# Kernel optimization log

Measured on AMD Instinct MI355X. Metric: run time of the kernel, lower is better.

## Reference

```python
import jax, jax.numpy as jnp
import numpy as np

NUM_HEADS = 16
HIDDEN = 1152
MLP = 4304
HEAD_DIM = HIDDEN // NUM_HEADS  # 72
SEQ = 3072
LN_EPS = 1e-5


def setup_inputs() -> dict:
    key = jax.random.key(0)
    ks = jax.random.split(key, 16)
    inv = 1.0 / np.sqrt(HIDDEN)
    inv_m = 1.0 / np.sqrt(MLP)
    pos = jnp.arange(SEQ, dtype=jnp.float32)[:, None]
    freq = jnp.exp(-jnp.arange(HEAD_DIM // 2, dtype=jnp.float32) * (np.log(10000.0) / (HEAD_DIM // 2)))
    ang = pos * freq[None, :]
    return {
        "hidden_states": jax.random.normal(ks[0], (SEQ, HIDDEN), jnp.float32),
        "rope_cos": jnp.cos(ang),
        "rope_sin": jnp.sin(ang),
        "ln0_g": jnp.ones((HIDDEN,), jnp.float32),
        "ln0_b": jnp.zeros((HIDDEN,), jnp.float32),
        "ln1_g": jnp.ones((HIDDEN,), jnp.float32),
        "ln1_b": jnp.zeros((HIDDEN,), jnp.float32),
        "wqkv_w": jax.random.normal(ks[1], (3 * HIDDEN, HIDDEN), jnp.float32) * inv,
        "wqkv_b": jnp.zeros((3 * HIDDEN,), jnp.float32),
        "wo_w": jax.random.normal(ks[2], (HIDDEN, HIDDEN), jnp.float32) * inv,
        "wo_b": jnp.zeros((HIDDEN,), jnp.float32),
        "fc0_w": jax.random.normal(ks[3], (MLP, HIDDEN), jnp.float32) * inv,
        "fc0_b": jnp.zeros((MLP,), jnp.float32),
        "fc1_w": jax.random.normal(ks[4], (HIDDEN, MLP), jnp.float32) * inv_m,
        "fc1_b": jnp.zeros((HIDDEN,), jnp.float32),
    }


def _layernorm(x, g, b):
    mu = jnp.mean(x, axis=-1, keepdims=True)
    var = jnp.mean(jnp.square(x - mu), axis=-1, keepdims=True)
    return (x - mu) * jax.lax.rsqrt(var + LN_EPS) * g + b


def _apply_rope(x, cos, sin):
    # x: [S, H, Dh]; cos/sin: [S, Dh/2]
    xp = x.astype(jnp.float32).reshape(*x.shape[:-1], -1, 2)  # [S, H, Dh/2, 2]
    xr, xi = xp[..., 0], xp[..., 1]
    c = cos[:, None, :]
    s = sin[:, None, :]
    out_r = xr * c - xi * s
    out_i = xr * s + xi * c
    return jnp.stack([out_r, out_i], axis=-1).reshape(x.shape).astype(x.dtype)


def reference(hidden_states, rope_cos, rope_sin, ln0_g, ln0_b, ln1_g, ln1_b,
              wqkv_w, wqkv_b, wo_w, wo_b, fc0_w, fc0_b, fc1_w, fc1_b):
    S = hidden_states.shape[0]
    residual = hidden_states
    h = _layernorm(hidden_states, ln0_g, ln0_b)
    xqkv = (h @ wqkv_w.T + wqkv_b).reshape(S, 3, NUM_HEADS, HEAD_DIM)
    xq, xk, xv = xqkv[:, 0], xqkv[:, 1], xqkv[:, 2]
    xq = _apply_rope(xq, rope_cos, rope_sin)
    xk = _apply_rope(xk, rope_cos, rope_sin)
    scale = 1.0 / np.sqrt(HEAD_DIM)
    scores = jnp.einsum('shd,thd->hst', xq, xk) * scale  # [H, S, S]
    attn = jax.nn.softmax(scores.astype(jnp.float32), axis=-1).astype(xq.dtype)
    out = jnp.einsum('hst,thd->shd', attn, xv).reshape(S, HIDDEN)
    h = residual + (out @ wo_w.T + wo_b)
    residual = h
    h = _layernorm(h, ln1_g, ln1_b)
    h = jax.nn.gelu(h @ fc0_w.T + fc0_b, approximate=True)
    h = h @ fc1_w.T + fc1_b
    return residual + h
```

## Files before the change

kernel.cpp:

```cpp
#include <hip/hip_runtime.h>
#include <hip/hip_bf16.h>
#include <math.h>

typedef __hip_bfloat16 bf16;
typedef __attribute__((ext_vector_type(8))) short short8;
typedef __attribute__((ext_vector_type(4))) short short4v;
typedef __attribute__((ext_vector_type(4))) float f32x4;

#define SEQ 3072
#define HID 1152
#define NHEAD 16
#define HD 72
#define HDP 96
#define MLPD 4304
#define MLPP 4352

__device__ __forceinline__ void async_lds16(void* lds, const void* g) {
  __builtin_amdgcn_global_load_lds((const __attribute__((address_space(1))) void*)g,
                                   (__attribute__((address_space(3))) void*)lds,
                                   16, 0, 0);
}

__device__ __forceinline__ unsigned cvt_pk2(float a, float b) {
  unsigned r;
  asm("v_cvt_pk_bf16_f32 %0, %1, %2" : "=v"(r) : "v"(a), "v"(b));
  return r;
}

__device__ __forceinline__ float exp2a(float x) {
  float r;
  asm("v_exp_f32 %0, %1" : "=v"(r) : "v"(x));
  return r;
}

__global__ __launch_bounds__(256) void cast_bf16_k(const float* __restrict__ in,
                                                   unsigned* __restrict__ out2, int n4) {
  int stride = gridDim.x * blockDim.x;
  for (int i = blockIdx.x * blockDim.x + threadIdx.x; i < n4; i += stride) {
    float4 u = ((const float4*)in)[i];
    uint2 w = make_uint2(cvt_pk2(u.x, u.y), cvt_pk2(u.z, u.w));
    ((uint2*)out2)[i] = w;
  }
}

__global__ __launch_bounds__(256) void cast_pad_rows_k(const float* __restrict__ in,
                                                       unsigned* __restrict__ out2,
                                                       int R, int C4, int n4) {
  int stride = gridDim.x * blockDim.x;
  for (int i = blockIdx.x * blockDim.x + threadIdx.x; i < n4; i += stride) {
    int r = i / C4;
    uint2 w = make_uint2(0u, 0u);
    if (r < R) {
      float4 u = ((const float4*)in)[i];
      w = make_uint2(cvt_pk2(u.x, u.y), cvt_pk2(u.z, u.w));
    }
    ((uint2*)out2)[i] = w;
  }
}

__global__ __launch_bounds__(256) void cast_pad_cols_k(const float* __restrict__ in,
                                                       unsigned* __restrict__ out2,
                                                       int C4, int Cp4, int n4) {
  int stride = gridDim.x * blockDim.x;
  for (int i = blockIdx.x * blockDim.x + threadIdx.x; i < n4; i += stride) {
    int r = i / Cp4, c4 = i - r * Cp4;
    uint2 w = make_uint2(0u, 0u);
    if (c4 < C4) {
      float4 u = ((const float4*)in)[r * C4 + c4];
      w = make_uint2(cvt_pk2(u.x, u.y), cvt_pk2(u.z, u.w));
    }
    ((uint2*)out2)[i] = w;
  }
}

__global__ __launch_bounds__(256) void ln_k(const float* __restrict__ x,
                                            const float* __restrict__ g,
                                            const float* __restrict__ b,
                                            bf16* __restrict__ o) {
  int row = blockIdx.x;
  const float4* xr = (const float4*)(x + (size_t)row * HID);
  float sum = 0.f, sq = 0.f;
  for (int c = threadIdx.x; c < HID / 4; c += 256) {
    float4 u = xr[c];
    sum += u.x + u.y + u.z + u.w;
    sq += u.x * u.x + u.y * u.y + u.z * u.z + u.w * u.w;
  }
#pragma unroll
  for (int off = 32; off > 0; off >>= 1) {
    sum += __shfl_down(sum, off, 64);
    sq += __shfl_down(sq, off, 64);
  }
  __shared__ float red[8];
  int wv = threadIdx.x >> 6;
  if ((threadIdx.x & 63) == 0) { red[wv] = sum; red[4 + wv] = sq; }
  __syncthreads();
  if (threadIdx.x == 0) {
    red[0] = red[0] + red[1] + red[2] + red[3];
    red[4] = red[4] + red[5] + red[6] + red[7];
  }
  __syncthreads();
  float mu = red[0] * (1.f / HID);
  float var = red[4] * (1.f / HID) - mu * mu;
  float inv = rsqrtf(var + 1e-5f);
  uint2* o4 = (uint2*)(o + (size_t)row * HID);
  const float4* g4 = (const float4*)g;
  const float4* b4 = (const float4*)b;
  for (int c = threadIdx.x; c < HID / 4; c += 256) {
    float4 u = xr[c], gg = g4[c], bb = b4[c];
    uint2 w = make_uint2(cvt_pk2((u.x - mu) * inv * gg.x + bb.x, (u.y - mu) * inv * gg.y + bb.y),
                         cvt_pk2((u.z - mu) * inv * gg.z + bb.z, (u.w - mu) * inv * gg.w + bb.w));
    o4[c] = w;
  }
}

template <int EPI>
__global__ __launch_bounds__(256) void gemm_bf16(const bf16* __restrict__ A,
                                                 const bf16* __restrict__ Bt,
                                                 const float* __restrict__ bias, int nbias,
                                                 const float* __restrict__ res,
                                                 float* __restrict__ outf,
                                                 bf16* __restrict__ outb,
                                                 int M, int N, int K) {
  __shared__ bf16 As[3][128 * 32];
  __shared__ bf16 Bs[3][128 * 32];
  const int t = threadIdx.x;
  const int l = t & 63;
  const int w = t >> 6;
  const int wr = w >> 1, wc = w & 1;
  const int lrow = l & 15;
  const int lk = (l >> 4) * 8;
  const int wg = (blockIdx.x & 7) * (gridDim.x >> 3) + (blockIdx.x >> 3);
  const int gyt = M >> 7;
  const int xt = wg / gyt;
  const int yt = wg - xt * gyt;
  const int m0 = yt * 128;
  const int n0 = xt * 128;
  const int arow = t >> 2;
  const int ach = (t & 3) * 8;

  const bf16* pa0 = &A[(size_t)(m0 + arow) * K + ach];
  const bf16* pa1 = &A[(size_t)(m0 + arow + 64) * K + ach];
  const bf16* pb0 = &Bt[(size_t)(n0 + arow) * K + ach];
  const bf16* pb1 = &Bt[(size_t)(n0 + arow + 64) * K + ach];
  auto STAGE = [&](int buf, int kt) {
    size_t off = (size_t)kt * 32;
    async_lds16(&As[buf][t * 8], pa0 + off);
    async_lds16(&As[buf][(256 + t) * 8], pa1 + off);
    async_lds16(&Bs[buf][t * 8], pb0 + off);
    async_lds16(&Bs[buf][(256 + t) * 8], pb1 + off);
  };

  f32x4 acc[4][4] = {};
  const int nkt = K >> 5;
  STAGE(0, 0);
  STAGE(1, 1);
  int bcur = 0;
  for (int kt = 0; kt < nkt; ++kt) {
    if (kt + 1 < nkt) {
      asm volatile("s_waitcnt vmcnt(4)" ::: "memory");
    } else {
      asm volatile("s_waitcnt vmcnt(0)" ::: "memory");
    }
    __builtin_amdgcn_s_barrier();
    int bn2 = bcur + 2;
    if (bn2 >= 3) bn2 -= 3;
    if (kt + 2 < nkt) STAGE(bn2, kt + 2);

    short8 af[4], bfr[4];
#pragma unroll
    for (int i = 0; i < 4; ++i)
      af[i] = *(const short8*)&As[bcur][(wr * 64 + i * 16 + lrow) * 32 + lk];
#pragma unroll
    for (int i = 0; i < 4; ++i)
      bfr[i] = *(const short8*)&Bs[bcur][(wc * 64 + i * 16 + lrow) * 32 + lk];
    __builtin_amdgcn_s_setprio(1);
#pragma unroll
    for (int i = 0; i < 4; ++i)
#pragma unroll
      for (int j = 0; j < 4; ++j)
        acc[i][j] = __builtin_amdgcn_mfma_f32_16x16x32_bf16(af[i], bfr[j], acc[i][j], 0, 0, 0);
    __builtin_amdgcn_s_setprio(0);
    ++bcur;
    if (bcur == 3) bcur = 0;
  }

#pragma unroll
  for (int i = 0; i < 4; ++i) {
    int rowb = m0 + wr * 64 + i * 16 + (l >> 4) * 4;
#pragma unroll
    for (int j = 0; j < 4; ++j) {
      int col = n0 + wc * 64 + j * 16 + lrow;
      float bv = (col < nbias) ? bias[col] : 0.f;
#pragma unroll
      for (int r2 = 0; r2 < 4; ++r2) {
        size_t idx = (size_t)(rowb + r2) * N + col;
        float v = acc[i][j][r2] + bv;
        if (EPI == 0) {
          outf[idx] = v;
        } else if (EPI == 1) {
          outf[idx] = v + res[idx];
        } else {
          float u = 0.7978845608028654f * (v + 0.044715f * v * v * v);
          u = fminf(fmaxf(u, -15.f), 15.f);
          float tt = __expf(2.f * u);
          outb[idx] = __float2bfloat16(v * tt / (tt + 1.f));
        }
      }
    }
  }
}

__global__ __launch_bounds__(256) void rope_split(const float* __restrict__ xqkv,
                                                  const float* __restrict__ cosb,
                                                  const float* __restrict__ sinb,
                                                  bf16* __restrict__ qp,
                                                  bf16* __restrict__ kp,
                                                  bf16* __restrict__ vt) {
  __shared__ bf16 vl[64][72];
  const int t = threadIdx.x;
  const int h = blockIdx.y;
  const int s0 = blockIdx.x * 64;
  const float scale = 0.17002445f;
  for (int idx = t; idx < 64 * 48; idx += 256) {
    int sl = idx / 48, pi = idx - sl * 48;
    int srow = s0 + sl;
    size_t obase = ((size_t)h * SEQ + srow) * HDP + 2 * pi;
    if (pi < 36) {
      const float* xr = xqkv + (size_t)srow * (3 * HID) + h * HD + 2 * pi;
      float qr = xr[0], qi = xr[1];
      float kr = xr[HID], ki = xr[HID + 1];
      float c = cosb[srow * 36 + pi], sn = sinb[srow * 36 + pi];
      *(unsigned*)&qp[obase] = cvt_pk2((qr * c - qi * sn) * scale, (qr * sn + qi * c) * scale);
      *(unsigned*)&kp[obase] = cvt_pk2(kr * c - ki * sn, kr * sn + ki * c);
    } else {
      *(unsigned*)&qp[obase] = 0u;
      *(unsigned*)&kp[obase] = 0u;
    }
  }
  for (int idx = t; idx < 64 * 72; idx += 256) {
    int sl = idx / 72, d = idx - sl * 72;
    vl[sl][d] = __float2bfloat16(xqkv[(size_t)(s0 + sl) * (3 * HID) + 2 * HID + h * HD + d]);
  }
  __syncthreads();
  bf16 z = __float2bfloat16(0.f);
  for (int idx = t; idx < HDP * 64; idx += 256) {
    int d = idx / 64, sl = idx - d * 64;
    vt[((size_t)h * HDP + d) * SEQ + s0 + sl] = (d < 72) ? vl[sl][d] : z;
  }
}

__global__ __launch_bounds__(128) void flash_attn(const bf16* __restrict__ q,
                                                  const bf16* __restrict__ kk,
                                                  const bf16* __restrict__ vT,
                                                  bf16* __restrict__ o) {
  __shared__ alignas(16) bf16 KV3[3 * 6144];
  __shared__ alignas(16) bf16 Pl[2][2][512];
  const int t = threadIdx.x;
  const int l = t & 63;
  const int w = t >> 6;
  const int g = l >> 4;
  const int lrow = l & 15;
  const int bid = blockIdx.x;
  const int kq = bid >> 3;
  const int h = (bid & 7) * 2 + (kq & 1);
  const int q0 = (kq >> 1) * 64 + w * 32;
  const int NT = SEQ / 32;

  const bf16* sbase[6];
  int smul[6];
#pragma unroll
  for (int i = 0; i < 6; ++i) {
    int s = t + i * 128;
    if (s < 384) {
      int cb = s >> 5, kv = s & 31;
      sbase[i] = kk + ((size_t)h * SEQ + kv) * HDP + cb * 8;
      smul[i] = 32 * HDP;
    } else {
      int vs = s - 384;
      int cb = vs / 96, d = vs - cb * 96;
      sbase[i] = vT + ((size_t)h * HDP + d) * SEQ + cb * 8;
      smul[i] = 32;
    }
  }
  auto STAGE = [&](int tile, int bufOff) {
#pragma unroll
    for (int i = 0; i < 6; ++i)
      async_lds16(&KV3[bufOff + (t + i * 128) * 8], sbase[i] + (size_t)tile * smul[i]);
  };

  short8 qf[2][3];
#pragma unroll
  for (int ss = 0; ss < 2; ++ss)
#pragma unroll
    for (int f = 0; f < 3; ++f)
      qf[ss][f] =
          *(const short8*)&q[((size_t)h * SEQ + q0 + ss * 16 + lrow) * HDP + f * 32 + g * 8];

  float m_r[2] = {-1e30f, -1e30f};
  float l_r[2] = {0.f, 0.f};
  f32x4 oa0[5] = {}, oa1[5] = {};

  STAGE(0, 0);
  STAGE(1, 6144);
  STAGE(2, 12288);
  asm volatile("s_waitcnt vmcnt(12)" ::: "memory");
  __builtin_amdgcn_s_barrier();

  f32x4 stA[2][2] = {}, stB[2][2];
  int b0 = 0;
#pragma unroll
  for (int nf = 0; nf < 2; ++nf)
#pragma unroll
    for (int f = 0; f < 3; ++f) {
      short8 kfrag = *(const short8*)&KV3[0 + (f * 4 + g) * 256 + (nf * 16 + lrow) * 8];
      stA[0][nf] = __builtin_amdgcn_mfma_f32_16x16x32_bf16(kfrag, qf[0][f], stA[0][nf], 0, 0, 0);
      stA[1][nf] = __builtin_amdgcn_mfma_f32_16x16x32_bf16(kfrag, qf[1][f], stA[1][nf], 0, 0, 0);
    }

  auto SOFTMAX = [&](f32x4* st, float& mr, float& lr, f32x4* oav, int ss) {
    float pmax = fmaxf(fmaxf(fmaxf(st[0][0], st[0][1]), fmaxf(st[0][2], st[0][3])),
                       fmaxf(fmaxf(st[1][0], st[1][1]), fmaxf(st[1][2], st[1][3])));
    if (!__all(pmax - mr <= 11.54f)) {
      float rm = pmax;
      rm = fmaxf(rm, __shfl_xor(rm, 16, 64));
      rm = fmaxf(rm, __shfl_xor(rm, 32, 64));
      float mn = fmaxf(mr, rm);
      float alpha = exp2a(mr - mn);
      lr *= alpha;
#pragma unroll
      for (int nf = 0; nf < 5; ++nf)
#pragma unroll
        for (int r = 0; r < 4; ++r) oav[nf][r] *= alpha;
      mr = mn;
    }
#pragma unroll
    for (int nf = 0; nf < 2; ++nf)
#pragma unroll
      for (int r = 0; r < 4; ++r) st[nf][r] = exp2a(st[nf][r] - mr);
    lr += (st[0][0] + st[0][1]) + (st[0][2] + st[0][3]) +
          (st[1][0] + st[1][1]) + (st[1][2] + st[1][3]);
#pragma unroll
    for (int nf = 0; nf < 2; ++nf) {
      uint2* dst = (uint2*)&Pl[w][ss][(2 * nf + (g >> 1)) * 128 + lrow * 8 + (g & 1) * 4];
      *dst = make_uint2(cvt_pk2(st[nf][0], st[nf][1]), cvt_pk2(st[nf][2], st[nf][3]));
    }
  };

  for (int kt = 0; kt < NT - 1; ++kt) {
    int b1 = b0 + 6144;
    if (b1 == 18432) b1 = 0;
    asm volatile("s_waitcnt vmcnt(6)" ::: "memory");
    __builtin_amdgcn_s_barrier();

#pragma unroll
    for (int s2 = 0; s2 < 2; ++s2)
#pragma unroll
      for (int nf = 0; nf < 2; ++nf) stB[s2][nf] = (f32x4){0.f, 0.f, 0.f, 0.f};
    __builtin_amdgcn_s_setprio(1);
#pragma unroll
    for (int nf = 0; nf < 2; ++nf)
#pragma unroll
      for (int f = 0; f < 3; ++f) {
        short8 kfrag = *(const short8*)&KV3[b1 + (f * 4 + g) * 256 + (nf * 16 + lrow) * 8];
        stB[0][nf] = __builtin_amdgcn_mfma_f32_16x16x32_bf16(kfrag, qf[0][f], stB[0][nf], 0, 0, 0);
        stB[1][nf] = __builtin_amdgcn_mfma_f32_16x16x32_bf16(kfrag, qf[1][f], stB[1][nf], 0, 0, 0);
      }
    __builtin_amdgcn_s_setprio(0);

    SOFTMAX(stA[0], m_r[0], l_r[0], oa0, 0);
    SOFTMAX(stA[1], m_r[1], l_r[1], oa1, 1);

    {
      short8 pa0 = *(const short8*)&Pl[w][0][g * 128 + lrow * 8];
      short8 pa1 = *(const short8*)&Pl[w][1][g * 128 + lrow * 8];
      __builtin_amdgcn_s_setprio(1);
#pragma unroll
      for (int nf = 0; nf < 5; ++nf) {
        short8 bv = *(const short8*)&KV3[b0 + 3072 + g * 768 + (nf * 16 + lrow) * 8];
        oa0[nf] = __builtin_amdgcn_mfma_f32_16x16x32_bf16(bv, pa0, oa0[nf], 0, 0, 0);
        oa1[nf] = __builtin_amdgcn_mfma_f32_16x16x32_bf16(bv, pa1, oa1[nf], 0, 0, 0);
      }
      __builtin_amdgcn_s_setprio(0);
    }

    asm volatile("s_waitcnt lgkmcnt(0)" ::: "memory");
    __builtin_amdgcn_s_barrier();
    int s = kt + 3;
    if (s >= NT) s -= NT;
    STAGE(s, b0);
#pragma unroll
    for (int s2 = 0; s2 < 2; ++s2)
#pragma unroll
      for (int nf = 0; nf < 2; ++nf) stA[s2][nf] = stB[s2][nf];
    b0 = b1;
  }

  SOFTMAX(stA[0], m_r[0], l_r[0], oa0, 0);
  SOFTMAX(stA[1], m_r[1], l_r[1], oa1, 1);
  {
    short8 pa0 = *(const short8*)&Pl[w][0][g * 128 + lrow * 8];
    short8 pa1 = *(const short8*)&Pl[w][1][g * 128 + lrow * 8];
#pragma unroll
    for (int nf = 0; nf < 5; ++nf) {
      short8 bv = *(const short8*)&KV3[b0 + 3072 + g * 768 + (nf * 16 + lrow) * 8];
      oa0[nf] = __builtin_amdgcn_mfma_f32_16x16x32_bf16(bv, pa0, oa0[nf], 0, 0, 0);
      oa1[nf] = __builtin_amdgcn_mfma_f32_16x16x32_bf16(bv, pa1, oa1[nf], 0, 0, 0);
    }
  }

#pragma unroll
  for (int ss = 0; ss < 2; ++ss) {
    f32x4* oav = ss ? oa1 : oa0;
    float lt = l_r[ss];
    lt += __shfl_xor(lt, 16, 64);
    lt += __shfl_xor(lt, 32, 64);
    float rcp = 1.f / lt;
    size_t obase = (size_t)(q0 + ss * 16 + lrow) * HID + h * HD;
#pragma unroll
    for (int nf = 0; nf < 5; ++nf) {
      int d = nf * 16 + g * 4;
      if (d + 3 < HD) {
        uint2 pk = make_uint2(cvt_pk2(oav[nf][0] * rcp, oav[nf][1] * rcp),
                              cvt_pk2(oav[nf][2] * rcp, oav[nf][3] * rcp));
        *(uint2*)&o[obase + d] = pk;
      }
    }
  }
}

extern "C" void kernel_launch(void* const* d_in, const int* in_sizes, int n_in,
                              void* d_out, int out_size, void* d_ws, size_t ws_size,
                              hipStream_t stream) {
  (void)in_sizes; (void)n_in; (void)out_size;
  const float* hidden = (const float*)d_in[0];
  const float* cosb = (const float*)d_in[1];
  const float* sinb = (const float*)d_in[2];
  const float* ln0g = (const float*)d_in[3];
  const float* ln0b = (const float*)d_in[4];
  const float* ln1g = (const float*)d_in[5];
  const float* ln1b = (const float*)d_in[6];
  const float* wqkv = (const float*)d_in[7];
  const float* bqkv = (const float*)d_in[8];
  const float* wo = (const float*)d_in[9];
  const float* bo = (const float*)d_in[10];
  const float* w0 = (const float*)d_in[11];
  const float* b0 = (const float*)d_in[12];
  const float* w1 = (const float*)d_in[13];
  const float* b1 = (const float*)d_in[14];

  char* p = (char*)d_ws;
  auto alloc = [&](size_t n) {
    char* r = p;
    p += (n + 255) & ~(size_t)255;
    return r;
  };
  bf16* wqkv_bf = (bf16*)alloc((size_t)3 * HID * HID * 2);
  bf16* wo_bf = (bf16*)alloc((size_t)HID * HID * 2);
  bf16* fc0_bf = (bf16*)alloc((size_t)MLPP * HID * 2);
  bf16* fc1_bf = (bf16*)alloc((size_t)HID * MLPP * 2);
  bf16* ln0_bf = (bf16*)alloc((size_t)SEQ * HID * 2);
  float* xqkv = (float*)alloc((size_t)SEQ * 3 * HID * 4);
  bf16* qp = (bf16*)alloc((size_t)NHEAD * SEQ * HDP * 2);
  bf16* kp = (bf16*)alloc((size_t)NHEAD * SEQ * HDP * 2);
  bf16* vt = (bf16*)alloc((size_t)NHEAD * HDP * SEQ * 2);
  bf16* attn_bf = (bf16*)alloc((size_t)SEQ * HID * 2);
  float* h1 = (float*)alloc((size_t)SEQ * HID * 4);
  bf16* ln1_bf = (bf16*)alloc((size_t)SEQ * HID * 2);
  bf16* gelu_bf = (bf16*)alloc((size_t)SEQ * MLPP * 2);
  if ((size_t)(p - (char*)d_ws) > ws_size) return;

  dim3 blk(256);
  cast_bf16_k<<<2048, blk, 0, stream>>>(wqkv, (unsigned*)wqkv_bf, 3 * HID * HID / 4);
  cast_bf16_k<<<1024, blk, 0, stream>>>(wo, (unsigned*)wo_bf, HID * HID / 4);
  cast_pad_rows_k<<<2048, blk, 0, stream>>>(w0, (unsigned*)fc0_bf, MLPD, HID / 4, MLPP * HID / 4);
  cast_pad_cols_k<<<2048, blk, 0, stream>>>(w1, (unsigned*)fc1_bf, MLPD / 4, MLPP / 4, HID * MLPP / 4);
  ln_k<<<SEQ, blk, 0, stream>>>(hidden, ln0g, ln0b, ln0_bf);
  gemm_bf16<0><<<dim3((3 * HID / 128) * (SEQ / 128)), blk, 0, stream>>>(
      ln0_bf, wqkv_bf, bqkv, 3 * HID, nullptr, xqkv, nullptr, SEQ, 3 * HID, HID);
  rope_split<<<dim3(SEQ / 64, NHEAD), blk, 0, stream>>>(xqkv, cosb, sinb, qp, kp, vt);
  flash_attn<<<dim3(768), dim3(128), 0, stream>>>(qp, kp, vt, attn_bf);
  gemm_bf16<1><<<dim3((HID / 128) * (SEQ / 128)), blk, 0, stream>>>(
      attn_bf, wo_bf, bo, HID, hidden, h1, nullptr, SEQ, HID, HID);
  ln_k<<<SEQ, blk, 0, stream>>>(h1, ln1g, ln1b, ln1_bf);
  gemm_bf16<2><<<dim3((MLPP / 128) * (SEQ / 128)), blk, 0, stream>>>(
      ln1_bf, fc0_bf, b0, MLPD, nullptr, nullptr, gelu_bf, SEQ, MLPP, HID);
  gemm_bf16<1><<<dim3((HID / 128) * (SEQ / 128)), blk, 0, stream>>>(
      gelu_bf, fc1_bf, b1, HID, h1, (float*)d_out, nullptr, SEQ, HID, MLPP);
}
```

Measured before the change: 399.9 us.

## Restructure flash attention to 6 waves × 16 rows with 64-wide KV tiles

The flash attention kernel moves from 2 waves each handling 32 query rows with 32-key tiles to 6 waves each handling 16 query rows with 64-key tiles. K and V get separate LDS buffers, triple-buffered for K and double-buffered for V, and the grid drops to 512 blocks of 384 threads. The aim is more reuse of each staged KV tile across query rows and fewer loop iterations and barriers. In exchange each wave keeps fewer query rows in flight, and a larger block coordinates on every barrier.

```diff
diff --git a/kernel.cpp b/kernel.cpp
--- a/kernel.cpp
+++ b/kernel.cpp
@@ -249,12 +249,13 @@
   }
 }
 
-__global__ __launch_bounds__(128) void flash_attn(const bf16* __restrict__ q,
+__global__ __launch_bounds__(384) void flash_attn(const bf16* __restrict__ q,
                                                   const bf16* __restrict__ kk,
                                                   const bf16* __restrict__ vT,
                                                   bf16* __restrict__ o) {
-  __shared__ alignas(16) bf16 KV3[3 * 6144];
-  __shared__ alignas(16) bf16 Pl[2][2][512];
+  __shared__ alignas(16) bf16 Ks[3][6144];
+  __shared__ alignas(16) bf16 Vs[2][6144];
+  __shared__ alignas(16) bf16 Pl[6][1024];
   const int t = threadIdx.x;
   const int l = t & 63;
   const int w = t >> 6;
@@ -263,167 +264,147 @@
   const int bid = blockIdx.x;
   const int kq = bid >> 3;
   const int h = (bid & 7) * 2 + (kq & 1);
-  const int q0 = (kq >> 1) * 64 + w * 32;
-  const int NT = SEQ / 32;
-
-  const bf16* sbase[6];
-  int smul[6];
-#pragma unroll
-  for (int i = 0; i < 6; ++i) {
-    int s = t + i * 128;
-    if (s < 384) {
-      int cb = s >> 5, kv = s & 31;
-      sbase[i] = kk + ((size_t)h * SEQ + kv) * HDP + cb * 8;
-      smul[i] = 32 * HDP;
-    } else {
-      int vs = s - 384;
-      int cb = vs / 96, d = vs - cb * 96;
-      sbase[i] = vT + ((size_t)h * HDP + d) * SEQ + cb * 8;
-      smul[i] = 32;
-    }
-  }
-  auto STAGE = [&](int tile, int bufOff) {
-#pragma unroll
-    for (int i = 0; i < 6; ++i)
-      async_lds16(&KV3[bufOff + (t + i * 128) * 8], sbase[i] + (size_t)tile * smul[i]);
-  };
-
-  short8 qf[2][3];
-#pragma unroll
-  for (int ss = 0; ss < 2; ++ss)
-#pragma unroll
-    for (int f = 0; f < 3; ++f)
-      qf[ss][f] =
-          *(const short8*)&q[((size_t)h * SEQ + q0 + ss * 16 + lrow) * HDP + f * 32 + g * 8];
-
-  float m_r[2] = {-1e30f, -1e30f};
-  float l_r[2] = {0.f, 0.f};
-  f32x4 oa0[5] = {}, oa1[5] = {};
-
-  STAGE(0, 0);
-  STAGE(1, 6144);
-  STAGE(2, 12288);
-  asm volatile("s_waitcnt vmcnt(12)" ::: "memory");
+  const int q0 = (kq >> 1) * 96 + w * 16;
+  const int NT = SEQ / 64;
+
+  const bf16* kbase[2];
+  const bf16* vbase[2];
+#pragma unroll
+  for (int i = 0; i < 2; ++i) {
+    int s = t + i * 384;
+    int cb = s >> 6, kv = s & 63;
+    kbase[i] = kk + ((size_t)h * SEQ + kv) * HDP + cb * 8;
+    int vs = t + i * 384;
+    int vcb = vs / 96, d = vs - vcb * 96;
+    vbase[i] = vT + ((size_t)h * HDP + d) * SEQ + vcb * 8;
+  }
+  auto STAGE_K = [&](int tile, int kb) {
+    size_t off = (size_t)tile * 64 * HDP;
+    async_lds16(&Ks[kb][t * 8], kbase[0] + off);
+    async_lds16(&Ks[kb][(t + 384) * 8], kbase[1] + off);
+  };
+  auto STAGE_V = [&](int tile, int vb) {
+    size_t off = (size_t)tile * 64;
+    async_lds16(&Vs[vb][t * 8], vbase[0] + off);
+    async_lds16(&Vs[vb][(t + 384) * 8], vbase[1] + off);
+  };
+
+  short8 qf[3];
+#pragma unroll
+  for (int f = 0; f < 3; ++f)
+    qf[f] = *(const short8*)&q[((size_t)h * SEQ + q0 + lrow) * HDP + f * 32 + g * 8];
+
+  float m_r = -1e30f, l_r = 0.f;
+  f32x4 oa[5] = {};
+
+  STAGE_K(0, 0);
+  STAGE_V(0, 0);
+  STAGE_K(1, 1);
+  STAGE_V(1, 1);
+  asm volatile("s_waitcnt vmcnt(6)" ::: "memory");
   __builtin_amdgcn_s_barrier();
 
-  f32x4 stA[2][2] = {}, stB[2][2];
-  int b0 = 0;
-#pragma unroll
-  for (int nf = 0; nf < 2; ++nf)
+  f32x4 stA[4] = {}, stB[4];
+#pragma unroll
+  for (int nf = 0; nf < 4; ++nf)
 #pragma unroll
     for (int f = 0; f < 3; ++f) {
-      short8 kfrag = *(const short8*)&KV3[0 + (f * 4 + g) * 256 + (nf * 16 + lrow) * 8];
-      stA[0][nf] = __builtin_amdgcn_mfma_f32_16x16x32_bf16(kfrag, qf[0][f], stA[0][nf], 0, 0, 0);
-      stA[1][nf] = __builtin_amdgcn_mfma_f32_16x16x32_bf16(kfrag, qf[1][f], stA[1][nf], 0, 0, 0);
-    }
-
-  auto SOFTMAX = [&](f32x4* st, float& mr, float& lr, f32x4* oav, int ss) {
-    float pmax = fmaxf(fmaxf(fmaxf(st[0][0], st[0][1]), fmaxf(st[0][2], st[0][3])),
-                       fmaxf(fmaxf(st[1][0], st[1][1]), fmaxf(st[1][2], st[1][3])));
-    if (!__all(pmax - mr <= 11.54f)) {
+      short8 kfrag = *(const short8*)&Ks[0][(f * 4 + g) * 512 + (nf * 16 + lrow) * 8];
+      stA[nf] = __builtin_amdgcn_mfma_f32_16x16x32_bf16(kfrag, qf[f], stA[nf], 0, 0, 0);
+    }
+
+  auto SOFTMAX = [&](f32x4* st) {
+    float pmax = -1e30f;
+#pragma unroll
+    for (int nf = 0; nf < 4; ++nf)
+      pmax = fmaxf(pmax, fmaxf(fmaxf(st[nf][0], st[nf][1]), fmaxf(st[nf][2], st[nf][3])));
+    if (!__all(pmax - m_r <= 11.54f)) {
       float rm = pmax;
       rm = fmaxf(rm, __shfl_xor(rm, 16, 64));
       rm = fmaxf(rm, __shfl_xor(rm, 32, 64));
-      float mn = fmaxf(mr, rm);
-      float alpha = exp2a(mr - mn);
-      lr *= alpha;
+      float mn = fmaxf(m_r, rm);
+      float alpha = exp2a(m_r - mn);
+      l_r *= alpha;
 #pragma unroll
       for (int nf = 0; nf < 5; ++nf)
 #pragma unroll
-        for (int r = 0; r < 4; ++r) oav[nf][r] *= alpha;
-      mr = mn;
-    }
-#pragma unroll
-    for (int nf = 0; nf < 2; ++nf)
-#pragma unroll
-      for (int r = 0; r < 4; ++r) st[nf][r] = exp2a(st[nf][r] - mr);
-    lr += (st[0][0] + st[0][1]) + (st[0][2] + st[0][3]) +
-          (st[1][0] + st[1][1]) + (st[1][2] + st[1][3]);
-#pragma unroll
-    for (int nf = 0; nf < 2; ++nf) {
-      uint2* dst = (uint2*)&Pl[w][ss][(2 * nf + (g >> 1)) * 128 + lrow * 8 + (g & 1) * 4];
+        for (int r = 0; r < 4; ++r) oa[nf][r] *= alpha;
+      m_r = mn;
+    }
+#pragma unroll
+    for (int nf = 0; nf < 4; ++nf) {
+#pragma unroll
+      for (int r = 0; r < 4; ++r) st[nf][r] = exp2a(st[nf][r] - m_r);
+      l_r += (st[nf][0] + st[nf][1]) + (st[nf][2] + st[nf][3]);
+    }
+#pragma unroll
+    for (int nf = 0; nf < 4; ++nf) {
+      uint2* dst = (uint2*)&Pl[w][(2 * nf + (g >> 1)) * 128 + lrow * 8 + (g & 1) * 4];
       *dst = make_uint2(cvt_pk2(st[nf][0], st[nf][1]), cvt_pk2(st[nf][2], st[nf][3]));
     }
   };
 
+  auto PV = [&](int vb) {
+    short8 pa0 = *(const short8*)&Pl[w][g * 128 + lrow * 8];
+    short8 pa1 = *(const short8*)&Pl[w][(4 + g) * 128 + lrow * 8];
+    __builtin_amdgcn_s_setprio(1);
+#pragma unroll
+    for (int nf = 0; nf < 5; ++nf) {
+      short8 bv0 = *(const short8*)&Vs[vb][g * 768 + (nf * 16 + lrow) * 8];
+      oa[nf] = __builtin_amdgcn_mfma_f32_16x16x32_bf16(bv0, pa0, oa[nf], 0, 0, 0);
+      short8 bv1 = *(const short8*)&Vs[vb][(4 + g) * 768 + (nf * 16 + lrow) * 8];
+      oa[nf] = __builtin_amdgcn_mfma_f32_16x16x32_bf16(bv1, pa1, oa[nf], 0, 0, 0);
+    }
+    __builtin_amdgcn_s_setprio(0);
+  };
+
   for (int kt = 0; kt < NT - 1; ++kt) {
-    int b1 = b0 + 6144;
-    if (b1 == 18432) b1 = 0;
-    asm volatile("s_waitcnt vmcnt(6)" ::: "memory");
+    asm volatile("s_waitcnt vmcnt(2)" ::: "memory");
     __builtin_amdgcn_s_barrier();
 
-#pragma unroll
-    for (int s2 = 0; s2 < 2; ++s2)
-#pragma unroll
-      for (int nf = 0; nf < 2; ++nf) stB[s2][nf] = (f32x4){0.f, 0.f, 0.f, 0.f};
+    const int kb1 = (kt + 1) % 3;
+#pragma unroll
+    for (int nf = 0; nf < 4; ++nf) stB[nf] = (f32x4){0.f, 0.f, 0.f, 0.f};
     __builtin_amdgcn_s_setprio(1);
 #pragma unroll
-    for (int nf = 0; nf < 2; ++nf)
+    for (int nf = 0; nf < 4; ++nf)
 #pragma unroll
       for (int f = 0; f < 3; ++f) {
-        short8 kfrag = *(const short8*)&KV3[b1 + (f * 4 + g) * 256 + (nf * 16 + lrow) * 8];
-        stB[0][nf] = __builtin_amdgcn_mfma_f32_16x16x32_bf16(kfrag, qf[0][f], stB[0][nf], 0, 0, 0);
-        stB[1][nf] = __builtin_amdgcn_mfma_f32_16x16x32_bf16(kfrag, qf[1][f], stB[1][nf], 0, 0, 0);
+        short8 kfrag = *(const short8*)&Ks[kb1][(f * 4 + g) * 512 + (nf * 16 + lrow) * 8];
+        stB[nf] = __builtin_amdgcn_mfma_f32_16x16x32_bf16(kfrag, qf[f], stB[nf], 0, 0, 0);
       }
     __builtin_amdgcn_s_setprio(0);
 
-    SOFTMAX(stA[0], m_r[0], l_r[0], oa0, 0);
-    SOFTMAX(stA[1], m_r[1], l_r[1], oa1, 1);
-
-    {
-      short8 pa0 = *(const short8*)&Pl[w][0][g * 128 + lrow * 8];
-      short8 pa1 = *(const short8*)&Pl[w][1][g * 128 + lrow * 8];
-      __builtin_amdgcn_s_setprio(1);
-#pragma unroll
-      for (int nf = 0; nf < 5; ++nf) {
-        short8 bv = *(const short8*)&KV3[b0 + 3072 + g * 768 + (nf * 16 + lrow) * 8];
-        oa0[nf] = __builtin_amdgcn_mfma_f32_16x16x32_bf16(bv, pa0, oa0[nf], 0, 0, 0);
-        oa1[nf] = __builtin_amdgcn_mfma_f32_16x16x32_bf16(bv, pa1, oa1[nf], 0, 0, 0);
-      }
-      __builtin_amdgcn_s_setprio(0);
-    }
+    SOFTMAX(stA);
+    PV(kt & 1);
 
     asm volatile("s_waitcnt lgkmcnt(0)" ::: "memory");
     __builtin_amdgcn_s_barrier();
-    int s = kt + 3;
+    int s = kt + 2;
     if (s >= NT) s -= NT;
-    STAGE(s, b0);
-#pragma unroll
-    for (int s2 = 0; s2 < 2; ++s2)
-#pragma unroll
-      for (int nf = 0; nf < 2; ++nf) stA[s2][nf] = stB[s2][nf];
-    b0 = b1;
-  }
-
-  SOFTMAX(stA[0], m_r[0], l_r[0], oa0, 0);
-  SOFTMAX(stA[1], m_r[1], l_r[1], oa1, 1);
-  {
-    short8 pa0 = *(const short8*)&Pl[w][0][g * 128 + lrow * 8];
-    short8 pa1 = *(const short8*)&Pl[w][1][g * 128 + lrow * 8];
-#pragma unroll
-    for (int nf = 0; nf < 5; ++nf) {
-      short8 bv = *(const short8*)&KV3[b0 + 3072 + g * 768 + (nf * 16 + lrow) * 8];
-      oa0[nf] = __builtin_amdgcn_mfma_f32_16x16x32_bf16(bv, pa0, oa0[nf], 0, 0, 0);
-      oa1[nf] = __builtin_amdgcn_mfma_f32_16x16x32_bf16(bv, pa1, oa1[nf], 0, 0, 0);
-    }
-  }
-
-#pragma unroll
-  for (int ss = 0; ss < 2; ++ss) {
-    f32x4* oav = ss ? oa1 : oa0;
-    float lt = l_r[ss];
-    lt += __shfl_xor(lt, 16, 64);
-    lt += __shfl_xor(lt, 32, 64);
-    float rcp = 1.f / lt;
-    size_t obase = (size_t)(q0 + ss * 16 + lrow) * HID + h * HD;
-#pragma unroll
-    for (int nf = 0; nf < 5; ++nf) {
-      int d = nf * 16 + g * 4;
-      if (d + 3 < HD) {
-        uint2 pk = make_uint2(cvt_pk2(oav[nf][0] * rcp, oav[nf][1] * rcp),
-                              cvt_pk2(oav[nf][2] * rcp, oav[nf][3] * rcp));
-        *(uint2*)&o[obase + d] = pk;
-      }
+    STAGE_K(s, (kt + 2) % 3);
+    STAGE_V(s, kt & 1);
+#pragma unroll
+    for (int nf = 0; nf < 4; ++nf) stA[nf] = stB[nf];
+  }
+
+  asm volatile("s_waitcnt vmcnt(4)" ::: "memory");
+  __builtin_amdgcn_s_barrier();
+  SOFTMAX(stA);
+  PV((NT - 1) & 1);
+
+  float lt = l_r;
+  lt += __shfl_xor(lt, 16, 64);
+  lt += __shfl_xor(lt, 32, 64);
+  float rcp = 1.f / lt;
+  size_t obase = (size_t)(q0 + lrow) * HID + h * HD;
+#pragma unroll
+  for (int nf = 0; nf < 5; ++nf) {
+    int d = nf * 16 + g * 4;
+    if (d + 3 < HD) {
+      uint2 pk = make_uint2(cvt_pk2(oa[nf][0] * rcp, oa[nf][1] * rcp),
+                            cvt_pk2(oa[nf][2] * rcp, oa[nf][3] * rcp));
+      *(uint2*)&o[obase + d] = pk;
     }
   }
 }
@@ -478,7 +459,7 @@
   gemm_bf16<0><<<dim3((3 * HID / 128) * (SEQ / 128)), blk, 0, stream>>>(
       ln0_bf, wqkv_bf, bqkv, 3 * HID, nullptr, xqkv, nullptr, SEQ, 3 * HID, HID);
   rope_split<<<dim3(SEQ / 64, NHEAD), blk, 0, stream>>>(xqkv, cosb, sinb, qp, kp, vt);
-  flash_attn<<<dim3(768), dim3(128), 0, stream>>>(qp, kp, vt, attn_bf);
+  flash_attn<<<dim3(512), dim3(384), 0, stream>>>(qp, kp, vt, attn_bf);
   gemm_bf16<1><<<dim3((HID / 128) * (SEQ / 128)), blk, 0, stream>>>(
       attn_bf, wo_bf, bo, HID, hidden, h1, nullptr, SEQ, HID, HID);
   ln_k<<<SEQ, blk, 0, stream>>>(h1, ln1g, ln1b, ln1_bf);
```

After: 424.5 us. 1.06x slower.
